# Kernel optimization log

Measured on AMD Instinct MI355X. Metric: run time of the kernel, lower is better.

Reference implementation:

```python
import jax, jax.numpy as jnp
import numpy as np

MARGIN = 1.0
NUM_CLASSES = 28
K = 16


def setup_inputs() -> dict:
    key = jax.random.key(0)
    k1, k2, k3 = jax.random.split(key, 3)
    B, C, D = 256, 28, 2048
    # multilabel prediction probabilities
    inp = jax.random.uniform(k1, (B, C), dtype=jnp.float32)
    # sparse multilabel targets (p~0.02 so minority-class selection via
    # cumsum(counts) <= 0.5*num_classes is non-degenerate)
    target = jax.random.bernoulli(k2, 0.02, (B, C)).astype(jnp.int32)
    # embeddings used for the mined triplets
    X = jax.random.normal(k3, (B, D), dtype=jnp.float32)
    return {"input": inp, "target": target, "X": X}


def _crl_loss(inp, X, target):
    B = inp.shape[0]
    y = target.astype(inp.dtype)

    # --- get_minority_classes ---
    counts = y.sum(0)                                   # [C] per-class positive counts
    order = jnp.argsort(counts)                         # ascending by count
    cum = jnp.cumsum(counts[order])
    keep_sorted = cum <= 0.5 * NUM_CLASSES              # threshold as in source
    rank = jnp.argsort(order)                           # position of class c in sorted order
    minority = keep_sorted[rank] & (counts > 1)         # [C] bool mask over classes

    # pairwise L1 distances between embeddings: Dm[i,j] = sum_d |X_i - X_j|
    Dm = jnp.abs(X[:, None, :] - X[None, :, :]).sum(-1)  # [B,B]

    pos_mask = target == 1                              # [B,C]
    inf = jnp.inf
    pos_key = jnp.where(pos_mask, inp, inf)             # [B,C] sort keys for positives
    neg_key = jnp.where(pos_mask, -inf, inp)            # [B,C] sort keys for negatives

    def per_class(pk, nk, pm, m_c):
        # hardest negatives of this class: largest predicted prob (neg_idxs[-k:])
        nvals, nidx = jax.lax.top_k(nk, K)              # [K]
        nvalid = jnp.isfinite(nvals).astype(Dm.dtype)
        n_n = nvalid.sum()                              # min(k, n_neg)
        dn_anchor = (Dm[:, nidx] * nvalid).sum(-1)      # [B] sum_j |X_i - X_negj|_1

        def per_anchor(i):
            keys = pk.at[i].set(inf)                    # mask[idx] = 0: exclude anchor
            # hardest positives: smallest predicted prob (sorted[:k])
            pvals, pidx = jax.lax.top_k(-keys, K)
            pvalid = jnp.isfinite(pvals).astype(Dm.dtype)
            n_p = pvalid.sum()                          # min(k, n_pos - 1)
            dp = (Dm[i, pidx] * pvalid).sum()
            w = (pm[i] & m_c).astype(Dm.dtype)          # anchor is a positive of a minority class
            # each positive appears in n_n triplets, each negative in n_p triplets
            return w * n_n * dp, w * n_p * dn_anchor[i]

        dps, dns = jax.vmap(per_anchor)(jnp.arange(B))
        return dps.sum(), dns.sum()

    dp_c, dn_c = jax.vmap(per_class, in_axes=(1, 1, 1, 0))(pos_key, neg_key, pos_mask, minority)
    # TripletLoss with F.l1_loss(size_average=False) sums over all triplet elements,
    # so distance_positive / distance_negative are scalars -> scalar relu loss.
    return jax.nn.relu(dp_c.sum() - dn_c.sum() + MARGIN)


def reference(input, target, X):
    return _crl_loss(input, X, target)
```

## Files before the change

### kernel.cpp

```cpp
#include <hip/hip_runtime.h>
#include <math.h>

typedef unsigned long long u64;
typedef unsigned int u32;

#define BB 256
#define CC 28
#define DD 2048
#define KK 16

__global__ __launch_bounds__(256) void k_main(const float* __restrict__ inp,
                                              const int* __restrict__ target,
                                              const float* __restrict__ X,
                                              float* __restrict__ part) {
  const int c = blockIdx.x;
  const int a = blockIdx.y;
  const int tid = threadIdx.x;
  const int wave = tid >> 6, lane = tid & 63;

  __shared__ u32 posbits[BB];
  __shared__ int s_cw[4][CC];
  __shared__ int s_counts[CC];
  __shared__ int s_N[KK];
  __shared__ int s_S[KK + 2];
  __shared__ int s_anchor;
  __shared__ float s_red[8];

  u32 pb = 0;
  const int4* t4 = (const int4*)(target + tid * CC);
#pragma unroll
  for (int k = 0; k < 7; ++k) {
    int4 w = t4[k];
    pb |= (u32)(w.x != 0) << (4 * k) | (u32)(w.y != 0) << (4 * k + 1) |
          (u32)(w.z != 0) << (4 * k + 2) | (u32)(w.w != 0) << (4 * k + 3);
  }
  posbits[tid] = pb;

#pragma unroll
  for (int c2 = 0; c2 < CC; ++c2) {
    u64 b = __ballot((pb >> c2) & 1u);
    if (lane == 0) s_cw[wave][c2] = __popcll(b);
  }
  __syncthreads();
  if (tid < CC)
    s_counts[tid] = s_cw[0][tid] + s_cw[1][tid] + s_cw[2][tid] + s_cw[3][tid];
  __syncthreads();

  const int m = s_counts[c];
  int cum = 0;
#pragma unroll
  for (int c2 = 0; c2 < CC; ++c2) {
    const int m2 = s_counts[c2];
    if (m2 < m || (m2 == m && c2 <= c)) cum += m2;
  }
  const bool active = (2 * cum <= CC) && (m > 1) && (a < m) && (a < KK);
  if (!active) {
    if (tid == 0) { part[2 * (c * KK + a)] = 0.f; part[2 * (c * KK + a) + 1] = 0.f; }
    return;
  }

  const int mS = min(m, KK + 1);
  const int NP = min(KK, m - 1);
  const int NN = min(KK, BB - m);

  if (wave == 0) {
    u64 kn[4];
#pragma unroll
    for (int q = 0; q < 4; ++q) {
      const int row = lane + 64 * q;
      const float val = inp[row * CC + c];
      const int p = (posbits[row] >> c) & 1;
      kn[q] = p ? 0ull
                : (((u64)__float_as_uint(val)) << 32) | (u64)(0xFFFFFFFFu - row);
    }
    for (int t = 0; t < KK; ++t) {
      u64 b = kn[0];
#pragma unroll
      for (int q = 1; q < 4; ++q) b = kn[q] > b ? kn[q] : b;
#pragma unroll
      for (int s = 1; s < 64; s <<= 1) {
        const u64 o = __shfl_xor(b, s);
        b = o > b ? o : b;
      }
      const int row = (int)(0xFFFFFFFFu - (u32)b);
      if (lane == 0) s_N[t] = row;
      if ((row & 63) == lane) kn[row >> 6] = 0ull;
    }
  } else if (wave == 1) {
    u64 kp[4];
#pragma unroll
    for (int q = 0; q < 4; ++q) {
      const int row = lane + 64 * q;
      const float val = inp[row * CC + c];
      const int p = (posbits[row] >> c) & 1;
      kp[q] = p ? (((u64)__float_as_uint(val)) << 32) | (u64)row
                : 0xFFFFFFFFFFFFFFFFull;
    }
    for (int t = 0; t < mS; ++t) {
      u64 b = kp[0];
#pragma unroll
      for (int q = 1; q < 4; ++q) b = kp[q] < b ? kp[q] : b;
#pragma unroll
      for (int s = 1; s < 64; s <<= 1) {
        const u64 o = __shfl_xor(b, s);
        b = o < b ? o : b;
      }
      const int row = (int)(u32)(b & 0xFFFFFFFFull);
      if (lane == 0) s_S[t] = row;
      if ((row & 63) == lane) kp[row >> 6] = 0xFFFFFFFFFFFFFFFFull;
    }
  } else if (wave == 2) {
    int sel[4], lc = 0;
#pragma unroll
    for (int q = 0; q < 4; ++q) {
      sel[q] = (posbits[4 * lane + q] >> c) & 1;
      lc += sel[q];
    }
    int pre = lc;
#pragma unroll
    for (int s = 1; s < 64; s <<= 1) {
      const int o = __shfl_up(pre, s);
      if (lane >= s) pre += o;
    }
    const int ex = pre - lc;
    if (a >= ex && a < ex + lc) {
      int need = a - ex;
#pragma unroll
      for (int q = 0; q < 4; ++q) {
        if (sel[q]) {
          if (need == 0) s_anchor = 4 * lane + q;
          need--;
        }
      }
    }
  }
  __syncthreads();

  const int anchor = s_anchor;
  int idx_a = 0;
  for (int t = 0; t < mS; ++t)
    if (s_S[t] == anchor) idx_a = t;

  const float4* Xa = (const float4*)(X + (size_t)anchor * DD);
  float4 A[8];
#pragma unroll
  for (int q = 0; q < 8; ++q) A[q] = Xa[q * 64 + lane];

  float dpw = 0.f, dnw = 0.f;
  for (int p = wave; p < NP + NN; p += 4) {
    const bool isdp = (p < NP);
    const int j = isdp ? s_S[p + (p >= idx_a ? 1 : 0)] : s_N[p - NP];
    const float4* Xj = (const float4*)(X + (size_t)j * DD);
    float partial = 0.f;
#pragma unroll
    for (int q = 0; q < 8; ++q) {
      const float4 b4 = Xj[q * 64 + lane];
      partial += fabsf(A[q].x - b4.x) + fabsf(A[q].y - b4.y) +
                 fabsf(A[q].z - b4.z) + fabsf(A[q].w - b4.w);
    }
#pragma unroll
    for (int s = 1; s < 64; s <<= 1) partial += __shfl_xor(partial, s);
    if (isdp) dpw += partial; else dnw += partial;
  }
  if (lane == 0) { s_red[2 * wave] = dpw; s_red[2 * wave + 1] = dnw; }
  __syncthreads();

  if (tid == 0) {
    const float dp = s_red[0] + s_red[2] + s_red[4] + s_red[6];
    const float dn = s_red[1] + s_red[3] + s_red[5] + s_red[7];
    part[2 * (c * KK + a)] = (float)NN * dp;
    part[2 * (c * KK + a) + 1] = (float)NP * dn;
  }
}

__global__ __launch_bounds__(256) void k_final(const float* __restrict__ part,
                                               float* __restrict__ out) {
  const int tid = threadIdx.x;
  const int wave = tid >> 6, lane = tid & 63;
  __shared__ float s_red[8];

  float dp = 0.f, dn = 0.f;
  for (int t = tid; t < CC * KK; t += 256) {
    dp += part[2 * t];
    dn += part[2 * t + 1];
  }
#pragma unroll
  for (int s = 1; s < 64; s <<= 1) {
    dp += __shfl_xor(dp, s);
    dn += __shfl_xor(dn, s);
  }
  if (lane == 0) { s_red[2 * wave] = dp; s_red[2 * wave + 1] = dn; }
  __syncthreads();
  if (tid == 0) {
    const float dpT = s_red[0] + s_red[2] + s_red[4] + s_red[6];
    const float dnT = s_red[1] + s_red[3] + s_red[5] + s_red[7];
    out[0] = fmaxf(dpT - dnT + 1.0f, 0.0f);
  }
}

extern "C" void kernel_launch(void* const* d_in, const int* in_sizes, int n_in,
                              void* d_out, int out_size, void* d_ws, size_t ws_size,
                              hipStream_t stream) {
  (void)in_sizes; (void)n_in; (void)out_size; (void)ws_size;
  const float* inp    = (const float*)d_in[0];
  const int*   target = (const int*)d_in[1];
  const float* X      = (const float*)d_in[2];
  float* out = (float*)d_out;
  float* part = (float*)d_ws;

  k_main<<<dim3(CC, KK), 256, 0, stream>>>(inp, target, X, part);
  k_final<<<1, 256, 0, stream>>>(part, out);
}
```

Before: 72.34 us.

## Split selection into per-class kernel and accumulate distances with atomics plus ticket

Moves the per-class positive/negative selection out of every anchor block into one selection kernel per class. It replaces the iterative wave-level top-k with a rank count per row. The distance kernel reads the precomputed lists, sums its contributions into global accumulators with atomics, and the last block (found through a ticket counter) writes the final relu, so the separate final-reduction kernel is gone. This removes the selection work that was repeated 16 times per class, at the cost of global-memory metadata traffic, atomics and a grid sized on the assumption that a minority class has at most 14 positives.

```diff
diff --git a/kernel.cpp b/kernel.cpp
--- a/kernel.cpp
+++ b/kernel.cpp
@@ -1,49 +1,63 @@
 #include <hip/hip_runtime.h>
 #include <math.h>
 
+typedef unsigned int u32;
 typedef unsigned long long u64;
-typedef unsigned int u32;
 
 #define BB 256
 #define CC 28
 #define DD 2048
 #define KK 16
+#define GA 14
+#define NBLK (CC * GA)
 
-__global__ __launch_bounds__(256) void k_main(const float* __restrict__ inp,
-                                              const int* __restrict__ target,
-                                              const float* __restrict__ X,
-                                              float* __restrict__ part) {
+struct Meta {
+  float acc[2];
+  u32 ticket;
+  u32 pad;
+  int active[CC];
+  int mcount[CC];
+  int alist[CC][16];
+  int slist[CC][16];
+  int nlist[CC][16];
+};
+
+__global__ __launch_bounds__(256) void k_sel(const float* __restrict__ inp,
+                                             const int* __restrict__ target,
+                                             Meta* __restrict__ M) {
   const int c = blockIdx.x;
-  const int a = blockIdx.y;
-  const int tid = threadIdx.x;
-  const int wave = tid >> 6, lane = tid & 63;
+  const int t = threadIdx.x;
+  const int wave = t >> 6, lane = t & 63;
 
-  __shared__ u32 posbits[BB];
+  __shared__ u32 s_bits[BB];
+  __shared__ u32 s_pb[BB];
   __shared__ int s_cw[4][CC];
   __shared__ int s_counts[CC];
-  __shared__ int s_N[KK];
-  __shared__ int s_S[KK + 2];
-  __shared__ int s_anchor;
-  __shared__ float s_red[8];
+  __shared__ int s_pw[4];
 
   u32 pb = 0;
-  const int4* t4 = (const int4*)(target + tid * CC);
+  const int4* t4 = (const int4*)(target + t * CC);
 #pragma unroll
   for (int k = 0; k < 7; ++k) {
     int4 w = t4[k];
     pb |= (u32)(w.x != 0) << (4 * k) | (u32)(w.y != 0) << (4 * k + 1) |
           (u32)(w.z != 0) << (4 * k + 2) | (u32)(w.w != 0) << (4 * k + 3);
   }
-  posbits[tid] = pb;
+  s_pb[t] = pb;
+  const float v = inp[t * CC + c];
+  s_bits[t] = __float_as_uint(v);
 
 #pragma unroll
   for (int c2 = 0; c2 < CC; ++c2) {
     u64 b = __ballot((pb >> c2) & 1u);
     if (lane == 0) s_cw[wave][c2] = __popcll(b);
   }
+  const int p = (pb >> c) & 1;
+  const u64 bp = __ballot(p != 0);
+  if (lane == 0) s_pw[wave] = __popcll(bp);
   __syncthreads();
-  if (tid < CC)
-    s_counts[tid] = s_cw[0][tid] + s_cw[1][tid] + s_cw[2][tid] + s_cw[3][tid];
+  if (t < CC)
+    s_counts[t] = s_cw[0][t] + s_cw[1][t] + s_cw[2][t] + s_cw[3][t];
   __syncthreads();
 
   const int m = s_counts[c];
@@ -51,150 +65,100 @@
 #pragma unroll
   for (int c2 = 0; c2 < CC; ++c2) {
     const int m2 = s_counts[c2];
-    if (m2 < m || (m2 == m && c2 <= c)) cum += m2;
+    cum += (m2 < m || (m2 == m && c2 <= c)) ? m2 : 0;
   }
-  const bool active = (2 * cum <= CC) && (m > 1) && (a < m) && (a < KK);
-  if (!active) {
-    if (tid == 0) { part[2 * (c * KK + a)] = 0.f; part[2 * (c * KK + a) + 1] = 0.f; }
-    return;
+  const bool active = (2 * cum <= CC) && (m > 1);
+
+  if (c == 0 && t == 0) { M->acc[0] = 0.f; M->acc[1] = 0.f; M->ticket = 0u; }
+  if (t == 0) { M->active[c] = active ? 1 : 0; M->mcount[c] = m; }
+  if (!active) return;
+
+  int rank = 0;
+  for (int j = 0; j < BB; ++j) {
+    const float vj = __uint_as_float(s_bits[j]);
+    const int pj = (s_pb[j] >> c) & 1;
+    const bool bpos = (vj < v) || (vj == v && j < t);
+    const bool bneg = (vj > v) || (vj == v && j < t);
+    rank += p ? ((pj && bpos) ? 1 : 0) : ((!pj && bneg) ? 1 : 0);
   }
-
-  const int mS = min(m, KK + 1);
-  const int NP = min(KK, m - 1);
-  const int NN = min(KK, BB - m);
-
-  if (wave == 0) {
-    u64 kn[4];
+  if (p) {
+    if (rank < 16) M->slist[c][rank] = t;
+    int idx = __popcll(bp & ((1ull << lane) - 1ull));
 #pragma unroll
-    for (int q = 0; q < 4; ++q) {
-      const int row = lane + 64 * q;
-      const float val = inp[row * CC + c];
-      const int p = (posbits[row] >> c) & 1;
-      kn[q] = p ? 0ull
-                : (((u64)__float_as_uint(val)) << 32) | (u64)(0xFFFFFFFFu - row);
-    }
-    for (int t = 0; t < KK; ++t) {
-      u64 b = kn[0];
-#pragma unroll
-      for (int q = 1; q < 4; ++q) b = kn[q] > b ? kn[q] : b;
-#pragma unroll
-      for (int s = 1; s < 64; s <<= 1) {
-        const u64 o = __shfl_xor(b, s);
-        b = o > b ? o : b;
-      }
-      const int row = (int)(0xFFFFFFFFu - (u32)b);
-      if (lane == 0) s_N[t] = row;
-      if ((row & 63) == lane) kn[row >> 6] = 0ull;
-    }
-  } else if (wave == 1) {
-    u64 kp[4];
-#pragma unroll
-    for (int q = 0; q < 4; ++q) {
-      const int row = lane + 64 * q;
-      const float val = inp[row * CC + c];
-      const int p = (posbits[row] >> c) & 1;
-      kp[q] = p ? (((u64)__float_as_uint(val)) << 32) | (u64)row
-                : 0xFFFFFFFFFFFFFFFFull;
-    }
-    for (int t = 0; t < mS; ++t) {
-      u64 b = kp[0];
-#pragma unroll
-      for (int q = 1; q < 4; ++q) b = kp[q] < b ? kp[q] : b;
-#pragma unroll
-      for (int s = 1; s < 64; s <<= 1) {
-        const u64 o = __shfl_xor(b, s);
-        b = o < b ? o : b;
-      }
-      const int row = (int)(u32)(b & 0xFFFFFFFFull);
-      if (lane == 0) s_S[t] = row;
-      if ((row & 63) == lane) kp[row >> 6] = 0xFFFFFFFFFFFFFFFFull;
-    }
-  } else if (wave == 2) {
-    int sel[4], lc = 0;
-#pragma unroll
-    for (int q = 0; q < 4; ++q) {
-      sel[q] = (posbits[4 * lane + q] >> c) & 1;
-      lc += sel[q];
-    }
-    int pre = lc;
-#pragma unroll
-    for (int s = 1; s < 64; s <<= 1) {
-      const int o = __shfl_up(pre, s);
-      if (lane >= s) pre += o;
-    }
-    const int ex = pre - lc;
-    if (a >= ex && a < ex + lc) {
-      int need = a - ex;
-#pragma unroll
-      for (int q = 0; q < 4; ++q) {
-        if (sel[q]) {
-          if (need == 0) s_anchor = 4 * lane + q;
-          need--;
-        }
-      }
-    }
-  }
-  __syncthreads();
-
-  const int anchor = s_anchor;
-  int idx_a = 0;
-  for (int t = 0; t < mS; ++t)
-    if (s_S[t] == anchor) idx_a = t;
-
-  const float4* Xa = (const float4*)(X + (size_t)anchor * DD);
-  float4 A[8];
-#pragma unroll
-  for (int q = 0; q < 8; ++q) A[q] = Xa[q * 64 + lane];
-
-  float dpw = 0.f, dnw = 0.f;
-  for (int p = wave; p < NP + NN; p += 4) {
-    const bool isdp = (p < NP);
-    const int j = isdp ? s_S[p + (p >= idx_a ? 1 : 0)] : s_N[p - NP];
-    const float4* Xj = (const float4*)(X + (size_t)j * DD);
-    float partial = 0.f;
-#pragma unroll
-    for (int q = 0; q < 8; ++q) {
-      const float4 b4 = Xj[q * 64 + lane];
-      partial += fabsf(A[q].x - b4.x) + fabsf(A[q].y - b4.y) +
-                 fabsf(A[q].z - b4.z) + fabsf(A[q].w - b4.w);
-    }
-#pragma unroll
-    for (int s = 1; s < 64; s <<= 1) partial += __shfl_xor(partial, s);
-    if (isdp) dpw += partial; else dnw += partial;
-  }
-  if (lane == 0) { s_red[2 * wave] = dpw; s_red[2 * wave + 1] = dnw; }
-  __syncthreads();
-
-  if (tid == 0) {
-    const float dp = s_red[0] + s_red[2] + s_red[4] + s_red[6];
-    const float dn = s_red[1] + s_red[3] + s_red[5] + s_red[7];
-    part[2 * (c * KK + a)] = (float)NN * dp;
-    part[2 * (c * KK + a) + 1] = (float)NP * dn;
+    for (int w2 = 0; w2 < 4; ++w2)
+      if (w2 < wave) idx += s_pw[w2];
+    if (idx < 16) M->alist[c][idx] = t;
+  } else {
+    if (rank < KK) M->nlist[c][rank] = t;
   }
 }
 
-__global__ __launch_bounds__(256) void k_final(const float* __restrict__ part,
-                                               float* __restrict__ out) {
+__global__ __launch_bounds__(256) void k_dist(const float* __restrict__ X,
+                                              Meta* __restrict__ M,
+                                              float* __restrict__ out) {
+  const int c = blockIdx.x;
+  const int a = blockIdx.y;
   const int tid = threadIdx.x;
   const int wave = tid >> 6, lane = tid & 63;
+
+  __shared__ int s_S[16], s_N[16];
   __shared__ float s_red[8];
 
-  float dp = 0.f, dn = 0.f;
-  for (int t = tid; t < CC * KK; t += 256) {
-    dp += part[2 * t];
-    dn += part[2 * t + 1];
+  const int m = M->mcount[c];
+  const bool work = (M->active[c] != 0) && (a < m);
+
+  if (work) {
+    if (tid < KK) s_N[tid] = M->nlist[c][tid];
+    else if (tid >= 64 && tid < 64 + m) s_S[tid - 64] = M->slist[c][tid - 64];
+    __syncthreads();
+
+    const int anchor = M->alist[c][a];
+    const int NP = m - 1;
+    const int NN = min(KK, BB - m);
+    int idx_a = 0;
+    for (int u = 0; u < m; ++u)
+      if (s_S[u] == anchor) idx_a = u;
+
+    const float4* Xa = (const float4*)(X + (size_t)anchor * DD);
+    float4 A[8];
+#pragma unroll
+    for (int q = 0; q < 8; ++q) A[q] = Xa[q * 64 + lane];
+
+    float dp = 0.f, dn = 0.f;
+    for (int pidx = wave; pidx < NP + NN; pidx += 4) {
+      const bool isdp = pidx < NP;
+      const int j = isdp ? s_S[pidx + (pidx >= idx_a ? 1 : 0)] : s_N[pidx - NP];
+      const float4* Xj = (const float4*)(X + (size_t)j * DD);
+      float partial = 0.f;
+#pragma unroll
+      for (int q = 0; q < 8; ++q) {
+        const float4 b4 = Xj[q * 64 + lane];
+        partial += fabsf(A[q].x - b4.x) + fabsf(A[q].y - b4.y) +
+                   fabsf(A[q].z - b4.z) + fabsf(A[q].w - b4.w);
+      }
+#pragma unroll
+      for (int s = 1; s < 64; s <<= 1) partial += __shfl_xor(partial, s);
+      if (isdp) dp += partial; else dn += partial;
+    }
+    if (lane == 0) { s_red[2 * wave] = dp; s_red[2 * wave + 1] = dn; }
+    __syncthreads();
+    if (tid == 0) {
+      const float dpT = s_red[0] + s_red[2] + s_red[4] + s_red[6];
+      const float dnT = s_red[1] + s_red[3] + s_red[5] + s_red[7];
+      atomicAdd(&M->acc[0], (float)NN * dpT);
+      atomicAdd(&M->acc[1], (float)NP * dnT);
+    }
   }
-#pragma unroll
-  for (int s = 1; s < 64; s <<= 1) {
-    dp += __shfl_xor(dp, s);
-    dn += __shfl_xor(dn, s);
-  }
-  if (lane == 0) { s_red[2 * wave] = dp; s_red[2 * wave + 1] = dn; }
-  __syncthreads();
+
   if (tid == 0) {
-    const float dpT = s_red[0] + s_red[2] + s_red[4] + s_red[6];
-    const float dnT = s_red[1] + s_red[3] + s_red[5] + s_red[7];
-    out[0] = fmaxf(dpT - dnT + 1.0f, 0.0f);
+    __threadfence();
+    const u32 tk = atomicAdd(&M->ticket, 1u);
+    if (tk == (u32)(NBLK - 1)) {
+      __threadfence();
+      const float a0 = atomicAdd(&M->acc[0], 0.f);
+      const float a1 = atomicAdd(&M->acc[1], 0.f);
+      out[0] = fmaxf(a0 - a1 + 1.0f, 0.0f);
+    }
   }
 }
 
@@ -206,8 +170,8 @@
   const int*   target = (const int*)d_in[1];
   const float* X      = (const float*)d_in[2];
   float* out = (float*)d_out;
-  float* part = (float*)d_ws;
+  Meta* M = (Meta*)d_ws;
 
-  k_main<<<dim3(CC, KK), 256, 0, stream>>>(inp, target, X, part);
-  k_final<<<1, 256, 0, stream>>>(part, out);
+  k_sel<<<CC, 256, 0, stream>>>(inp, target, M);
+  k_dist<<<dim3(CC, GA), 256, 0, stream>>>(X, M, out);
 }
```

Measured after the change: 85.32 us. +17.9%, slower.
